# Kernel optimization log

Measured on AMD Instinct MI355X. Metric: run time of the kernel, lower is better.

## Reference

```python
import jax, jax.numpy as jnp
import numpy as np

ROUTINGS = 3

def squash(v):
    # v: [..., D]
    n = jnp.linalg.norm(v, axis=-1, keepdims=True)
    n2 = n * n
    return (n2 / (1.0 + n2)) * v / (n + 1e-8)

def setup_inputs() -> dict:
    key = jax.random.key(0)
    k1, k2 = jax.random.split(key)
    B, O, I, D_out, D_in = 64, 32, 512, 64, 64
    x = jax.random.normal(k1, (B, I, D_in), dtype=jnp.float32)
    # xavier_uniform with gain=1.141 over last two dims (out_dim, in_dim)
    fan_in, fan_out = D_in, D_out
    bound = 1.141 * np.sqrt(6.0 / (fan_in + fan_out))
    weight = jax.random.uniform(k2, (O, I, D_out, D_in), dtype=jnp.float32,
                                minval=-bound, maxval=bound)
    return {"x": x, "weight": weight}

def reference(x, weight):
    # x: [B, I, D_in]; weight: [O, I, D_out, D_in]
    B = x.shape[0]
    O, I = weight.shape[0], weight.shape[1]
    # x_hat[b,o,i,d] = sum_m W[o,i,d,m] x[b,i,m]  -> [B, O, I, D_out]
    x_hat = jnp.einsum('oidm,bim->boid', weight, x)
    x_hat_detach = jax.lax.stop_gradient(x_hat)
    b = jnp.zeros((B, O, I), dtype=x.dtype)
    out = None
    for i in range(ROUTINGS):
        c = jax.nn.softmax(b, axis=1)  # softmax over out_num
        if i == ROUTINGS - 1:
            out = squash(jnp.einsum('boi,boid->bod', c, x_hat))
        else:
            out = squash(jnp.einsum('boi,boid->bod', c, x_hat_detach))
            # agreement: [B,O,I,D] . [B,O,D] -> [B,O,I]
            b = b + jnp.einsum('boid,bod->boi', x_hat_detach, out)
    return out  # [B, O, D_out]
```

## Files before the change

kernel.cpp:

```cpp
#include <hip/hip_runtime.h>
#include <stdint.h>

#define NB 64
#define NO 32
#define NI 512
#define ND 64

typedef __attribute__((ext_vector_type(8))) short short8;
typedef __attribute__((ext_vector_type(4))) float f32x4;

__device__ __forceinline__ float blo(unsigned int u) {
    union { unsigned int i; float f; } v; v.i = u << 16; return v.f;
}
__device__ __forceinline__ float bhi(unsigned int u) {
    union { unsigned int i; float f; } v; v.i = u & 0xFFFF0000u; return v.f;
}
__device__ __forceinline__ unsigned short f2bf(float f) {
    union { float f; unsigned int i; } v; v.f = f;
    return (unsigned short)((v.i + 0x7FFFu + ((v.i >> 16) & 1u)) >> 16);
}
__device__ __forceinline__ short8 pack8(const float4 a, const float4 b) {
    short8 r;
    r[0] = (short)f2bf(a.x); r[1] = (short)f2bf(a.y);
    r[2] = (short)f2bf(a.z); r[3] = (short)f2bf(a.w);
    r[4] = (short)f2bf(b.x); r[5] = (short)f2bf(b.y);
    r[6] = (short)f2bf(b.z); r[7] = (short)f2bf(b.w);
    return r;
}

__device__ __forceinline__ void ld_a(float4 r[4], const float* __restrict__ p) {
    r[0] = *(const float4*)(p);
    r[1] = *(const float4*)(p + 4);
    r[2] = *(const float4*)(p + 32);
    r[3] = *(const float4*)(p + 36);
}
__device__ __forceinline__ void ld_b(float4 r[16], const float* __restrict__ p) {
    #pragma unroll
    for (int td = 0; td < 4; ++td) {
        r[4 * td + 0] = *(const float4*)(p + td * 1024);
        r[4 * td + 1] = *(const float4*)(p + td * 1024 + 4);
        r[4 * td + 2] = *(const float4*)(p + td * 1024 + 32);
        r[4 * td + 3] = *(const float4*)(p + td * 1024 + 36);
    }
}

__global__ __launch_bounds__(256) void k_gemm(const float* __restrict__ x,
                                              const float* __restrict__ w,
                                              unsigned short* __restrict__ xh) {
    const int o  = blockIdx.x & 31;
    const int ig = blockIdx.x >> 5;
    const int t  = threadIdx.x;
    const int wv = t >> 6;
    const int l  = t & 63;
    const int q  = l >> 4;
    const int c  = l & 15;

    const float* ap0 = x + ((size_t)(16 * wv + c) * NI + ig * 8) * 64 + q * 8;
    const float* bp0 = w + ((size_t)o * NI + ig * 8) * 4096 + (size_t)c * 64 + q * 8;

    float4 ra[4], rb[16], na[4], nb[16];
    ld_a(ra, ap0);
    ld_b(rb, bp0);

    #pragma unroll
    for (int ii = 0; ii < 8; ++ii) {
        if (ii < 7) {
            ld_a(na, ap0 + (ii + 1) * 64);
            ld_b(nb, bp0 + (size_t)(ii + 1) * 4096);
        }
        const int i = ig * 8 + ii;
        const short8 a0 = pack8(ra[0], ra[1]);
        const short8 a1 = pack8(ra[2], ra[3]);
        f32x4 acc[4];
        #pragma unroll
        for (int td = 0; td < 4; ++td) {
            const short8 b0 = pack8(rb[4 * td + 0], rb[4 * td + 1]);
            const short8 b1 = pack8(rb[4 * td + 2], rb[4 * td + 3]);
            f32x4 z = {0.f, 0.f, 0.f, 0.f};
            z = __builtin_amdgcn_mfma_f32_16x16x32_bf16(a0, b0, z, 0, 0, 0);
            z = __builtin_amdgcn_mfma_f32_16x16x32_bf16(a1, b1, z, 0, 0, 0);
            acc[td] = z;
        }
        #pragma unroll
        for (int td = 0; td < 4; ++td) {
            const int d = 16 * td + c;
            #pragma unroll
            for (int r = 0; r < 4; ++r) {
                const int b = 16 * wv + 4 * q + r;
                xh[(((size_t)o * NB + b) * NI + i) * ND + d] = f2bf(acc[td][r]);
            }
        }
        #pragma unroll
        for (int j = 0; j < 4; ++j)  ra[j] = na[j];
        #pragma unroll
        for (int j = 0; j < 16; ++j) rb[j] = nb[j];
    }
}

template<int STEP>
__global__ __launch_bounds__(256) void k_route(const unsigned short* __restrict__ xh,
                                               const float* __restrict__ b_in,
                                               float* __restrict__ b_out,
                                               float* __restrict__ outp) {
    __shared__ float c_s[NI];
    __shared__ float P[4 * 64];
    __shared__ float o_s[64];

    const int t  = threadIdx.x;
    const int b  = blockIdx.x >> 5;
    const int o  = blockIdx.x & 31;
    const int dg = t & 7;
    const int ip = t >> 3;

    const unsigned short* gsrc = xh + ((size_t)o * NB + b) * NI * ND;
    uint4 raw[16];
    #pragma unroll
    for (int k = 0; k < 16; ++k)
        raw[k] = *(const uint4*)(gsrc + (size_t)(32 * k + ip) * ND + dg * 8);

    const float* bp = (STEP > 0) ? (b_in + (size_t)b * (NO * NI)) : nullptr;
    if (STEP > 0) {
        #pragma unroll
        for (int s = 0; s < 2; ++s) {
            const int i = t + s * 256;
            float m = -INFINITY, Z = 0.f;
            #pragma unroll
            for (int oo = 0; oo < NO; ++oo) {
                const float v = bp[(size_t)oo * NI + i];
                const float nm = fmaxf(m, v);
                Z = Z * __expf(m - nm) + __expf(v - nm);
                m = nm;
            }
            c_s[i] = __expf(bp[(size_t)o * NI + i] - m) / Z;
        }
        __syncthreads();
    }

    float acc[8] = {0, 0, 0, 0, 0, 0, 0, 0};
    #pragma unroll
    for (int k = 0; k < 16; ++k) {
        const float cw = (STEP == 0) ? 0.03125f : c_s[32 * k + ip];
        acc[0] += cw * blo(raw[k].x); acc[1] += cw * bhi(raw[k].x);
        acc[2] += cw * blo(raw[k].y); acc[3] += cw * bhi(raw[k].y);
        acc[4] += cw * blo(raw[k].z); acc[5] += cw * bhi(raw[k].z);
        acc[6] += cw * blo(raw[k].w); acc[7] += cw * bhi(raw[k].w);
    }
    #pragma unroll
    for (int j = 0; j < 8; ++j) {
        acc[j] += __shfl_xor(acc[j], 8);
        acc[j] += __shfl_xor(acc[j], 16);
        acc[j] += __shfl_xor(acc[j], 32);
    }
    const int lane = t & 63;
    const int wv = t >> 6;
    if (lane < 8) {
        #pragma unroll
        for (int j = 0; j < 8; ++j) P[wv * 64 + lane * 8 + j] = acc[j];
    }
    __syncthreads();

    if (t < 64) {
        const float sv = P[t] + P[64 + t] + P[128 + t] + P[192 + t];
        float s2 = sv * sv;
        #pragma unroll
        for (int m = 1; m < 64; m <<= 1) s2 += __shfl_xor(s2, m);
        const float n = sqrtf(s2);
        const float sc = (s2 / (1.0f + s2)) / (n + 1e-8f);
        const float ov = sv * sc;
        o_s[t] = ov;
        if (STEP == 2) outp[((size_t)b * NO + o) * ND + t] = ov;
    }
    __syncthreads();

    if (STEP < 2) {
        float oc[8];
        #pragma unroll
        for (int j = 0; j < 8; ++j) oc[j] = o_s[dg * 8 + j];
        float w1 = 0.f, w2 = 0.f;
        #pragma unroll
        for (int k = 0; k < 16; ++k) {
            float pd = blo(raw[k].x) * oc[0] + bhi(raw[k].x) * oc[1]
                     + blo(raw[k].y) * oc[2] + bhi(raw[k].y) * oc[3]
                     + blo(raw[k].z) * oc[4] + bhi(raw[k].z) * oc[5]
                     + blo(raw[k].w) * oc[6] + bhi(raw[k].w) * oc[7];
            pd += __shfl_xor(pd, 1);
            pd += __shfl_xor(pd, 2);
            pd += __shfl_xor(pd, 4);
            if (k == dg)     w1 = pd;
            if (k == dg + 8) w2 = pd;
        }
        const int i1 = 32 * dg + ip;
        const int i2 = 32 * (dg + 8) + ip;
        float* bo = b_out + ((size_t)b * NO + o) * NI;
        const float own1 = (STEP == 0) ? 0.f : bp[(size_t)o * NI + i1];
        const float own2 = (STEP == 0) ? 0.f : bp[(size_t)o * NI + i2];
        bo[i1] = own1 + w1;
        bo[i2] = own2 + w2;
    }
}

extern "C" void kernel_launch(void* const* d_in, const int* in_sizes, int n_in,
                              void* d_out, int out_size, void* d_ws, size_t ws_size,
                              hipStream_t stream) {
    const float* x = (const float*)d_in[0];
    const float* w = (const float*)d_in[1];
    float* outp = (float*)d_out;

    char* ws = (char*)d_ws;
    unsigned short* xh = (unsigned short*)ws;
    float* ba = (float*)(ws + (size_t)134217728);
    float* bb = (float*)(ws + (size_t)134217728 + 4194304);

    k_gemm<<<dim3(2048), dim3(256), 0, stream>>>(x, w, xh);
    k_route<0><<<dim3(2048), dim3(256), 0, stream>>>(xh, nullptr, ba, nullptr);
    k_route<1><<<dim3(2048), dim3(256), 0, stream>>>(xh, ba, bb, nullptr);
    k_route<2><<<dim3(2048), dim3(256), 0, stream>>>(xh, bb, nullptr, outp);
}
```

Before: 530.5 us.

## Stage weights via LDS DMA, precompute softmax stats, load routing tiles into LDS

The GEMM kernel now streams each weight slab into a triple-buffered, XOR-swizzled LDS ring using global_load_lds, replacing per-thread register prefetch. Loads become coalesced and register pressure drops, at the cost of a barrier per iteration. A small k_soft kernel computes the per-(b,i) softmax max and reciprocal sum once, so each routing block no longer re-reads all 32 logits per column. The routing kernels DMA their 64KB xh tile into dynamic LDS instead of holding it in 16 uint4 registers, which adds two launches and lowers occupancy through heavy LDS use.

```diff
diff --git a/kernel.cpp b/kernel.cpp
--- a/kernel.cpp
+++ b/kernel.cpp
@@ -8,6 +8,10 @@
 
 typedef __attribute__((ext_vector_type(8))) short short8;
 typedef __attribute__((ext_vector_type(4))) float f32x4;
+
+#define GL2LDS(g, s) __builtin_amdgcn_global_load_lds( \
+    (const __attribute__((address_space(1))) void*)(g), \
+    (__attribute__((address_space(3))) void*)(s), 16, 0, 0)
 
 __device__ __forceinline__ float blo(unsigned int u) {
     union { unsigned int i; float f; } v; v.i = u << 16; return v.f;
@@ -27,26 +31,17 @@
     r[6] = (short)f2bf(b.z); r[7] = (short)f2bf(b.w);
     return r;
 }
-
 __device__ __forceinline__ void ld_a(float4 r[4], const float* __restrict__ p) {
     r[0] = *(const float4*)(p);
     r[1] = *(const float4*)(p + 4);
     r[2] = *(const float4*)(p + 32);
     r[3] = *(const float4*)(p + 36);
 }
-__device__ __forceinline__ void ld_b(float4 r[16], const float* __restrict__ p) {
-    #pragma unroll
-    for (int td = 0; td < 4; ++td) {
-        r[4 * td + 0] = *(const float4*)(p + td * 1024);
-        r[4 * td + 1] = *(const float4*)(p + td * 1024 + 4);
-        r[4 * td + 2] = *(const float4*)(p + td * 1024 + 32);
-        r[4 * td + 3] = *(const float4*)(p + td * 1024 + 36);
-    }
-}
 
 __global__ __launch_bounds__(256) void k_gemm(const float* __restrict__ x,
                                               const float* __restrict__ w,
                                               unsigned short* __restrict__ xh) {
+    __shared__ float Wl[3][4096];
     const int o  = blockIdx.x & 31;
     const int ig = blockIdx.x >> 5;
     const int t  = threadIdx.x;
@@ -55,27 +50,45 @@
     const int q  = l >> 4;
     const int c  = l & 15;
 
+    const float* wbase = w + ((size_t)o * NI + ig * 8) * 4096;
+
+    auto stage = [&](int buf, int ii) {
+        const float* src = wbase + (size_t)ii * 4096;
+        #pragma unroll
+        for (int k = 0; k < 4; ++k) {
+            const int s = wv * 256 + k * 64 + l;
+            const int r = s >> 4;
+            const int g = (s & 15) ^ (r & 15);
+            GL2LDS(src + r * 64 + g * 4, &Wl[buf][(wv * 256 + k * 64) * 4]);
+        }
+    };
+
     const float* ap0 = x + ((size_t)(16 * wv + c) * NI + ig * 8) * 64 + q * 8;
-    const float* bp0 = w + ((size_t)o * NI + ig * 8) * 4096 + (size_t)c * 64 + q * 8;
-
-    float4 ra[4], rb[16], na[4], nb[16];
+    float4 ra[4], na[4];
     ld_a(ra, ap0);
-    ld_b(rb, bp0);
+    stage(0, 0);
+    stage(1, 1);
 
     #pragma unroll
     for (int ii = 0; ii < 8; ++ii) {
-        if (ii < 7) {
-            ld_a(na, ap0 + (ii + 1) * 64);
-            ld_b(nb, bp0 + (size_t)(ii + 1) * 4096);
-        }
+        __syncthreads();
+        if (ii < 6) stage((ii + 2) % 3, ii + 2);
+        if (ii < 7) ld_a(na, ap0 + (ii + 1) * 64);
+
         const int i = ig * 8 + ii;
+        const float* Wb = Wl[ii % 3];
         const short8 a0 = pack8(ra[0], ra[1]);
         const short8 a1 = pack8(ra[2], ra[3]);
         f32x4 acc[4];
         #pragma unroll
         for (int td = 0; td < 4; ++td) {
-            const short8 b0 = pack8(rb[4 * td + 0], rb[4 * td + 1]);
-            const short8 b1 = pack8(rb[4 * td + 2], rb[4 * td + 3]);
+            const int r = 16 * td + c;
+            const float4 f0 = *(const float4*)&Wb[(r * 16 + ((2 * q)     ^ c)) * 4];
+            const float4 f1 = *(const float4*)&Wb[(r * 16 + ((2 * q + 1) ^ c)) * 4];
+            const float4 f2 = *(const float4*)&Wb[(r * 16 + ((2 * q + 8) ^ c)) * 4];
+            const float4 f3 = *(const float4*)&Wb[(r * 16 + ((2 * q + 9) ^ c)) * 4];
+            const short8 b0 = pack8(f0, f1);
+            const short8 b1 = pack8(f2, f3);
             f32x4 z = {0.f, 0.f, 0.f, 0.f};
             z = __builtin_amdgcn_mfma_f32_16x16x32_bf16(a0, b0, z, 0, 0, 0);
             z = __builtin_amdgcn_mfma_f32_16x16x32_bf16(a1, b1, z, 0, 0, 0);
@@ -85,23 +98,42 @@
         for (int td = 0; td < 4; ++td) {
             const int d = 16 * td + c;
             #pragma unroll
-            for (int r = 0; r < 4; ++r) {
-                const int b = 16 * wv + 4 * q + r;
-                xh[(((size_t)o * NB + b) * NI + i) * ND + d] = f2bf(acc[td][r]);
+            for (int rr = 0; rr < 4; ++rr) {
+                const int b = 16 * wv + 4 * q + rr;
+                xh[(((size_t)o * NB + b) * NI + i) * ND + d] = f2bf(acc[td][rr]);
             }
         }
         #pragma unroll
-        for (int j = 0; j < 4; ++j)  ra[j] = na[j];
-        #pragma unroll
-        for (int j = 0; j < 16; ++j) rb[j] = nb[j];
-    }
+        for (int j = 0; j < 4; ++j) ra[j] = na[j];
+    }
+}
+
+__global__ __launch_bounds__(256) void k_soft(const float* __restrict__ b_in,
+                                              float* __restrict__ mz) {
+    const int p = blockIdx.x * 256 + threadIdx.x;
+    const int b = p >> 9, i = p & 511;
+    const float* bp = b_in + (size_t)b * NO * NI + i;
+    float v[NO];
+    #pragma unroll
+    for (int oo = 0; oo < NO; ++oo) v[oo] = bp[(size_t)oo * NI];
+    float m = v[0];
+    #pragma unroll
+    for (int oo = 1; oo < NO; ++oo) m = fmaxf(m, v[oo]);
+    float Z = 0.f;
+    #pragma unroll
+    for (int oo = 0; oo < NO; ++oo) Z += __expf(v[oo] - m);
+    mz[p] = m;
+    mz[NB * NI + p] = 1.0f / Z;
 }
 
 template<int STEP>
 __global__ __launch_bounds__(256) void k_route(const unsigned short* __restrict__ xh,
                                                const float* __restrict__ b_in,
+                                               const float* __restrict__ mz,
                                                float* __restrict__ b_out,
                                                float* __restrict__ outp) {
+    extern __shared__ char smem[];
+    unsigned short* tile = (unsigned short*)smem;
     __shared__ float c_s[NI];
     __shared__ float P[4 * 64];
     __shared__ float o_s[64];
@@ -109,41 +141,39 @@
     const int t  = threadIdx.x;
     const int b  = blockIdx.x >> 5;
     const int o  = blockIdx.x & 31;
+    const int wv = t >> 6;
+    const int l  = t & 63;
     const int dg = t & 7;
     const int ip = t >> 3;
 
     const unsigned short* gsrc = xh + ((size_t)o * NB + b) * NI * ND;
-    uint4 raw[16];
-    #pragma unroll
-    for (int k = 0; k < 16; ++k)
-        raw[k] = *(const uint4*)(gsrc + (size_t)(32 * k + ip) * ND + dg * 8);
-
-    const float* bp = (STEP > 0) ? (b_in + (size_t)b * (NO * NI)) : nullptr;
+    #pragma unroll
+    for (int k = 0; k < 16; ++k) {
+        GL2LDS(gsrc + wv * 8192 + k * 512 + l * 8, tile + wv * 8192 + k * 512);
+    }
+
+    const float* bp = (STEP > 0) ? (b_in + ((size_t)b * NO + o) * NI) : nullptr;
     if (STEP > 0) {
+        const float* mrow = mz + (size_t)b * NI;
+        const float* zrow = mz + (size_t)(NB * NI) + (size_t)b * NI;
         #pragma unroll
         for (int s = 0; s < 2; ++s) {
             const int i = t + s * 256;
-            float m = -INFINITY, Z = 0.f;
-            #pragma unroll
-            for (int oo = 0; oo < NO; ++oo) {
-                const float v = bp[(size_t)oo * NI + i];
-                const float nm = fmaxf(m, v);
-                Z = Z * __expf(m - nm) + __expf(v - nm);
-                m = nm;
-            }
-            c_s[i] = __expf(bp[(size_t)o * NI + i] - m) / Z;
-        }
-        __syncthreads();
-    }
+            c_s[i] = __expf(bp[i] - mrow[i]) * zrow[i];
+        }
+    }
+    __syncthreads();
 
     float acc[8] = {0, 0, 0, 0, 0, 0, 0, 0};
     #pragma unroll
     for (int k = 0; k < 16; ++k) {
-        const float cw = (STEP == 0) ? 0.03125f : c_s[32 * k + ip];
-        acc[0] += cw * blo(raw[k].x); acc[1] += cw * bhi(raw[k].x);
-        acc[2] += cw * blo(raw[k].y); acc[3] += cw * bhi(raw[k].y);
-        acc[4] += cw * blo(raw[k].z); acc[5] += cw * bhi(raw[k].z);
-        acc[6] += cw * blo(raw[k].w); acc[7] += cw * bhi(raw[k].w);
+        const int i = 32 * k + ip;
+        const uint4 raw = *(const uint4*)(tile + i * ND + dg * 8);
+        const float cw = (STEP == 0) ? 0.03125f : c_s[i];
+        acc[0] += cw * blo(raw.x); acc[1] += cw * bhi(raw.x);
+        acc[2] += cw * blo(raw.y); acc[3] += cw * bhi(raw.y);
+        acc[4] += cw * blo(raw.z); acc[5] += cw * bhi(raw.z);
+        acc[6] += cw * blo(raw.w); acc[7] += cw * bhi(raw.w);
     }
     #pragma unroll
     for (int j = 0; j < 8; ++j) {
@@ -151,11 +181,9 @@
         acc[j] += __shfl_xor(acc[j], 16);
         acc[j] += __shfl_xor(acc[j], 32);
     }
-    const int lane = t & 63;
-    const int wv = t >> 6;
-    if (lane < 8) {
-        #pragma unroll
-        for (int j = 0; j < 8; ++j) P[wv * 64 + lane * 8 + j] = acc[j];
+    if (l < 8) {
+        #pragma unroll
+        for (int j = 0; j < 8; ++j) P[wv * 64 + l * 8 + j] = acc[j];
     }
     __syncthreads();
 
@@ -179,10 +207,11 @@
         float w1 = 0.f, w2 = 0.f;
         #pragma unroll
         for (int k = 0; k < 16; ++k) {
-            float pd = blo(raw[k].x) * oc[0] + bhi(raw[k].x) * oc[1]
-                     + blo(raw[k].y) * oc[2] + bhi(raw[k].y) * oc[3]
-                     + blo(raw[k].z) * oc[4] + bhi(raw[k].z) * oc[5]
-                     + blo(raw[k].w) * oc[6] + bhi(raw[k].w) * oc[7];
+            const uint4 raw = *(const uint4*)(tile + (32 * k + ip) * ND + dg * 8);
+            float pd = blo(raw.x) * oc[0] + bhi(raw.x) * oc[1]
+                     + blo(raw.y) * oc[2] + bhi(raw.y) * oc[3]
+                     + blo(raw.z) * oc[4] + bhi(raw.z) * oc[5]
+                     + blo(raw.w) * oc[6] + bhi(raw.w) * oc[7];
             pd += __shfl_xor(pd, 1);
             pd += __shfl_xor(pd, 2);
             pd += __shfl_xor(pd, 4);
@@ -192,10 +221,8 @@
         const int i1 = 32 * dg + ip;
         const int i2 = 32 * (dg + 8) + ip;
         float* bo = b_out + ((size_t)b * NO + o) * NI;
-        const float own1 = (STEP == 0) ? 0.f : bp[(size_t)o * NI + i1];
-        const float own2 = (STEP == 0) ? 0.f : bp[(size_t)o * NI + i2];
-        bo[i1] = own1 + w1;
-        bo[i2] = own2 + w2;
+        bo[i1] = ((STEP == 0) ? 0.f : bp[i1]) + w1;
+        bo[i2] = ((STEP == 0) ? 0.f : bp[i2]) + w2;
     }
 }
 
@@ -210,9 +237,20 @@
     unsigned short* xh = (unsigned short*)ws;
     float* ba = (float*)(ws + (size_t)134217728);
     float* bb = (float*)(ws + (size_t)134217728 + 4194304);
+    float* mz = (float*)(ws + (size_t)134217728 + 2 * 4194304);
+
+    const int smem = 65536;
+    hipFuncSetAttribute(reinterpret_cast<const void*>(&k_route<0>),
+                        hipFuncAttributeMaxDynamicSharedMemorySize, smem);
+    hipFuncSetAttribute(reinterpret_cast<const void*>(&k_route<1>),
+                        hipFuncAttributeMaxDynamicSharedMemorySize, smem);
+    hipFuncSetAttribute(reinterpret_cast<const void*>(&k_route<2>),
+                        hipFuncAttributeMaxDynamicSharedMemorySize, smem);
 
     k_gemm<<<dim3(2048), dim3(256), 0, stream>>>(x, w, xh);
-    k_route<0><<<dim3(2048), dim3(256), 0, stream>>>(xh, nullptr, ba, nullptr);
-    k_route<1><<<dim3(2048), dim3(256), 0, stream>>>(xh, ba, bb, nullptr);
-    k_route<2><<<dim3(2048), dim3(256), 0, stream>>>(xh, bb, nullptr, outp);
-}
+    k_route<0><<<dim3(2048), dim3(256), smem, stream>>>(xh, nullptr, nullptr, ba, nullptr);
+    k_soft<<<dim3(128), dim3(256), 0, stream>>>(ba, mz);
+    k_route<1><<<dim3(2048), dim3(256), smem, stream>>>(xh, ba, mz, bb, nullptr);
+    k_soft<<<dim3(128), dim3(256), 0, stream>>>(bb, mz);
+    k_route<2><<<dim3(2048), dim3(256), smem, stream>>>(xh, bb, mz, nullptr, outp);
+}
```

Measured after the change: 487.0 us. -8.2%, faster.
